# Kernel tuning notes

Hardware: AMD Instinct MI355X
Metric: run time of the kernel (lower is better)

The kernel has to match this reference:

```python
import jax, jax.numpy as jnp
import numpy as np


def _interp1d(xq, yq, xnew):
    """torchinterp1d semantics: linear interp with end-slope extrapolation.
    xq: (Q,) nondecreasing knots, yq: (Q,) values, xnew: any shape."""
    ind = jnp.clip(jnp.searchsorted(xq, xnew), 1, xq.shape[0] - 1)
    x0 = xq[ind - 1]
    x1 = xq[ind]
    y0 = yq[ind - 1]
    y1 = yq[ind]
    return y0 + (y1 - y0) / (x1 - x0) * (xnew - x0)


def setup_inputs() -> dict:
    key = jax.random.key(0)
    k1, k2 = jax.random.split(key)
    x = jax.random.normal(k1, (64, 512, 2048), dtype=jnp.float32)  # (N, C, L)
    target_quantiles = jax.random.uniform(k2, (256,), dtype=jnp.float32)  # sorted inside reference, as in the module
    return {"x": x, "target_quantiles": target_quantiles}


def reference(x, target_quantiles):
    # BatchOT forward (training=True, batchwise_matching=True, smoothing=None).
    C = x.shape[1]
    xt = jnp.moveaxis(x, 1, -1)        # (N, ..., C)
    flat = xt.reshape(-1, C)           # (M, C)
    Q = target_quantiles.shape[0]
    qs = jnp.linspace(0.0, 1.0, Q, dtype=x.dtype)      # buffer `quantiles`
    # per-feature batch quantiles, torch.quantile default 'linear' interpolation
    sq = jnp.quantile(flat, qs, axis=0)                # (Q, C)
    sq = jnp.sort(sq, axis=0)
    tq = jnp.sort(target_quantiles)
    # 1) map data through inverse source quantile fn, per feature: (M, C) -> [0,1]
    u = jax.vmap(_interp1d, in_axes=(1, None, 1), out_axes=1)(sq, qs, flat)
    u = jnp.clip(u, 0.0, 1.0)
    # 2) map quantile levels through the target quantile function (shared knots)
    y = _interp1d(qs, tq, u)           # (M, C)
    y = y.reshape(xt.shape)
    return jnp.moveaxis(y, -1, 1)      # (N, C, ...)
```

## Files before the change

kernel.cpp:

```cpp
#include <hip/hip_runtime.h>
#include <stdint.h>

#define N_   64
#define C_   512
#define L_   2048
#define M_   131072
#define Q_   256
#define NR_  512
#define NL_  (C_ * L_)
#define CAP_ 7168

__device__ __forceinline__ uint32_t f2u(float f) {
    uint32_t u = __float_as_uint(f);
    return u ^ ((uint32_t)((int32_t)u >> 31) | 0x80000000u);
}
__device__ __forceinline__ float u2f(uint32_t u) {
    uint32_t v = (u & 0x80000000u) ? (u ^ 0x80000000u) : ~u;
    return __uint_as_float(v);
}
__device__ __forceinline__ uint32_t h0pad(uint32_t b) { return b + (b >> 5); }

__global__ void sort_tq_kernel(const float* __restrict__ tq_in, float* __restrict__ tq_out) {
    __shared__ float s[Q_];
    int t = threadIdx.x;
    s[t] = tq_in[t];
    __syncthreads();
    for (int k = 2; k <= Q_; k <<= 1) {
        for (int j = k >> 1; j > 0; j >>= 1) {
            int ixj = t ^ j;
            if (ixj > t) {
                float a = s[t], b = s[ixj];
                bool up = ((t & k) == 0);
                if ((a > b) == up) { s[t] = b; s[ixj] = a; }
            }
            __syncthreads();
        }
    }
    tq_out[t] = s[t];
}

__device__ __forceinline__ uint32_t waveScan(uint32_t v, int lane) {
    #pragma unroll
    for (int off = 1; off < 64; off <<= 1) {
        uint32_t t = __shfl_up(v, off, 64);
        if (lane >= off) v += t;
    }
    return v;
}
__device__ __forceinline__ uint32_t blockScan(uint32_t v, uint32_t* wsum, int tid) {
    const int lane = tid & 63, wid = tid >> 6;
    uint32_t s = waveScan(v, lane);
    if (lane == 63) wsum[wid] = s;
    __syncthreads();
    if (wid == 0) {
        uint32_t w = (lane < 16) ? wsum[lane] : 0u;
        w = waveScan(w, lane);
        if (lane < 16) wsum[lane] = w;
    }
    __syncthreads();
    uint32_t r = s + ((wid > 0) ? wsum[wid - 1] : 0u);
    __syncthreads();
    return r;
}

__device__ __forceinline__ uint32_t dedupe512(uint32_t* keys, uint32_t* wsum, uint32_t* gout,
                                              uint32_t mykey, int tid, uint32_t* headOut) {
    if (tid < NR_) keys[tid] = mykey;
    __syncthreads();
    uint32_t h = 0;
    if (tid < NR_) h = (tid == 0) ? 1u : ((keys[tid] != keys[tid - 1]) ? 1u : 0u);
    uint32_t incl = blockScan(h, wsum, tid);
    if (tid == NR_ - 1) *gout = incl;
    *headOut = h;
    return incl - 1u;
}

__device__ __forceinline__ uint32_t rank_walk8(const uint32_t* rows, uint32_t slot, uint32_t& lrnk) {
    uint32_t acc = 0, dig = 0;
    bool found = false;
    const uint32_t* r = rows + slot * 17u;
    #pragma unroll
    for (int w = 0; w < 16; ++w) {
        uint32_t word = r[w];
        #pragma unroll
        for (int b = 0; b < 4; ++b) {
            uint32_t cnt = (word >> (8 * b)) & 255u;
            if (!found) {
                if (acc + cnt > lrnk) { dig = 4u * w + b; found = true; } else acc += cnt;
            }
        }
    }
    lrnk -= acc;
    return dig;
}

#define SM_KEYS 16896
#define SM_WSUM 17408
#define SM_M1   17424
#define SM_BS1  18448
#define SM_CNT2 18960
#define SM_BASE 19472
#define SM_GC   19984
#define SM_WORDS 19988

__global__ __launch_bounds__(1024, 8) void qsel_kernel(const float* __restrict__ x,
                                                       const float* __restrict__ tqs,
                                                       float* __restrict__ out) {
    __shared__ uint32_t smem[SM_WORDS];
    uint32_t* hist0   = smem;
    uint32_t* selBit  = smem;
    uint32_t* selBase = smem + 512;
    uint32_t* rows    = smem + 1024;
    uint32_t* candK   = smem + 1024;
    uint32_t* candS   = smem + 8192;
    float*    ssq     = (float*)(smem + 1024);
    float*    stq     = (float*)(smem + 1280);
    uint16_t* tbl16   = (uint16_t*)(smem + 2048);
    uint32_t* keys    = smem + SM_KEYS;
    uint32_t* wsum    = smem + SM_WSUM;
    uint2*    m1      = (uint2*)(smem + SM_M1);
    uint32_t* bs1     = smem + SM_BS1;
    uint32_t* cnt2    = smem + SM_CNT2;
    uint32_t* base    = smem + SM_BASE;
    uint32_t* gc      = smem + SM_GC;

    const int c = blockIdx.x, tid = threadIdx.x;
    const float* xc = x + (size_t)c * L_;
    float*       oc = out + (size_t)c * L_;
    const int l4 = (tid & 511) << 2;
    const int n0 = tid >> 9;

    uint32_t lrnk = 0;
    if (tid < NR_) {
        int k = tid >> 1;
        float pos = ((float)k / 255.0f) * 131071.0f;
        int lo = (int)floorf(pos);
        if (lo > M_ - 1) lo = M_ - 1;
        if (lo < 0) lo = 0;
        int r = (tid & 1) ? ((lo + 1 > M_ - 1) ? M_ - 1 : lo + 1) : lo;
        lrnk = (uint32_t)r;
    }

    for (int i = tid; i < 16896; i += 1024) hist0[i] = 0u;
    if (tid < 4) gc[tid] = 0u;
    __syncthreads();
    for (int nn = n0; nn < N_; nn += 8) {
        float4 a = *reinterpret_cast<const float4*>(xc + (size_t)nn       * NL_ + l4);
        float4 b = *reinterpret_cast<const float4*>(xc + (size_t)(nn + 2) * NL_ + l4);
        float4 d = *reinterpret_cast<const float4*>(xc + (size_t)(nn + 4) * NL_ + l4);
        float4 e = *reinterpret_cast<const float4*>(xc + (size_t)(nn + 6) * NL_ + l4);
        float vv[16] = {a.x,a.y,a.z,a.w, b.x,b.y,b.z,b.w, d.x,d.y,d.z,d.w, e.x,e.y,e.z,e.w};
        #pragma unroll
        for (int q = 0; q < 16; ++q)
            atomicAdd(&hist0[h0pad(f2u(vv[q]) >> 18)], 1u);
    }
    __syncthreads();

    {
        uint32_t bb = (uint32_t)tid * 16u; bb += (bb >> 5);
        uint32_t acc = 0;
        #pragma unroll
        for (int i = 0; i < 16; ++i) { acc += hist0[bb + i]; hist0[bb + i] = acc; }
        uint32_t excl = blockScan(acc, wsum, tid) - acc;
        #pragma unroll
        for (int i = 0; i < 16; ++i) hist0[bb + i] += excl;
    }
    __syncthreads();

    uint32_t mykey = 0;
    if (tid < NR_) {
        uint32_t d = 0;
        #pragma unroll
        for (uint32_t s = 8192; s > 0; s >>= 1)
            if (d + s <= 16384u && hist0[h0pad(d + s - 1u)] <= lrnk) d += s;
        uint32_t below = d ? hist0[h0pad(d - 1u)] : 0u;
        mykey = d;
        lrnk -= below;
    }
    __syncthreads();

    uint32_t head;
    uint32_t slot = dedupe512(keys, wsum, gc + 0, mykey, tid, &head);
    __syncthreads();

    if (tid < 512) { selBit[tid] = 0u; selBase[tid] = 0u; m1[tid] = make_uint2(0u, 0u); }
    for (int i = 1024 + tid; i < 9728; i += 1024) smem[i] = 0u;
    __syncthreads();
    if (tid < NR_ && head) atomicOr(&selBit[mykey >> 5], 1u << (mykey & 31u));
    __syncthreads();
    {
        uint32_t pc = (tid < 512) ? __popc(selBit[tid]) : 0u;
        uint32_t incl = blockScan(pc, wsum, tid);
        if (tid < 512) selBase[tid] = incl - pc;
    }
    __syncthreads();

    for (int nn = n0; nn < N_; nn += 8) {
        float4 a = *reinterpret_cast<const float4*>(xc + (size_t)nn       * NL_ + l4);
        float4 b = *reinterpret_cast<const float4*>(xc + (size_t)(nn + 2) * NL_ + l4);
        float4 d = *reinterpret_cast<const float4*>(xc + (size_t)(nn + 4) * NL_ + l4);
        float4 e = *reinterpret_cast<const float4*>(xc + (size_t)(nn + 6) * NL_ + l4);
        float vv[16] = {a.x,a.y,a.z,a.w, b.x,b.y,b.z,b.w, d.x,d.y,d.z,d.w, e.x,e.y,e.z,e.w};
        #pragma unroll
        for (int q = 0; q < 16; ++q) {
            uint32_t key = f2u(vv[q]);
            uint32_t bin = key >> 18;
            uint32_t w = selBit[bin >> 5];
            uint32_t bt = bin & 31u;
            if ((w >> bt) & 1u) {
                uint32_t slt = selBase[bin >> 5] + __popc(w & ((1u << bt) - 1u));
                uint32_t dd = (key >> 12) & 63u;
                atomicAdd(&rows[slt * 17u + (dd >> 2)], 1u << ((dd & 3u) << 3));
            }
        }
    }
    __syncthreads();

    uint32_t dig = 0;
    if (tid < NR_) { dig = rank_walk8(rows, slot, lrnk); mykey = (mykey << 6) | dig; }
    __syncthreads();
    uint32_t head1;
    uint32_t g1 = dedupe512(keys, wsum, gc + 1, mykey, tid, &head1);
    if (tid < NR_ && head1)
        atomicOr(&((uint32_t*)m1)[2u * slot + (dig >> 5)], 1u << (dig & 31u));
    if (tid == 0) gc[2] = 0u;
    if (tid < 512) cnt2[tid] = 0u;
    __syncthreads();
    {
        uint32_t S = gc[0];
        uint32_t pc = (tid < (int)S) ? (__popc(m1[tid].x) + __popc(m1[tid].y)) : 0u;
        uint32_t incl = blockScan(pc, wsum, tid);
        if (tid < 512) bs1[tid] = incl - pc;
    }
    __syncthreads();

    for (int nn = n0; nn < N_; nn += 8) {
        float4 a = *reinterpret_cast<const float4*>(xc + (size_t)nn       * NL_ + l4);
        float4 b = *reinterpret_cast<const float4*>(xc + (size_t)(nn + 2) * NL_ + l4);
        float4 d = *reinterpret_cast<const float4*>(xc + (size_t)(nn + 4) * NL_ + l4);
        float4 e = *reinterpret_cast<const float4*>(xc + (size_t)(nn + 6) * NL_ + l4);
        float vv[16] = {a.x,a.y,a.z,a.w, b.x,b.y,b.z,b.w, d.x,d.y,d.z,d.w, e.x,e.y,e.z,e.w};
        #pragma unroll
        for (int q = 0; q < 16; ++q) {
            uint32_t key = f2u(vv[q]);
            uint32_t bin = key >> 18;
            uint32_t w = selBit[bin >> 5];
            uint32_t bt = bin & 31u;
            if (!((w >> bt) & 1u)) continue;
            uint32_t slt = selBase[bin >> 5] + __popc(w & ((1u << bt) - 1u));
            uint2 mm = m1[slt];
            uint32_t dd = (key >> 12) & 63u;
            uint32_t mw = (dd < 32u) ? mm.x : mm.y;
            uint32_t db = dd & 31u;
            if (!((mw >> db) & 1u)) continue;
            uint32_t g = bs1[slt] + ((dd < 32u) ? __popc(mm.x & ((1u << db) - 1u))
                                                : __popc(mm.x) + __popc(mm.y & ((1u << db) - 1u)));
            uint32_t pos = atomicAdd(&gc[2], 1u);
            if (pos < CAP_) candK[pos] = key;
            atomicAdd(&cnt2[g], 1u);
        }
    }
    __syncthreads();

    uint32_t G1 = gc[1];
    uint32_t total = gc[2]; if (total > CAP_) total = CAP_;
    {
        uint32_t cv = (tid < (int)G1) ? cnt2[tid] : 0u;
        uint32_t incl = blockScan(cv, wsum, tid);
        if (tid < 512) { base[tid] = incl - cv; cnt2[tid] = 0u; }
    }
    __syncthreads();
    for (int i = tid; i < (int)total; i += 1024) {
        uint32_t key = candK[i];
        uint32_t bin = key >> 18;
        uint32_t w = selBit[bin >> 5];
        uint32_t bt = bin & 31u;
        uint32_t slt = selBase[bin >> 5] + __popc(w & ((1u << bt) - 1u));
        uint2 mm = m1[slt];
        uint32_t dd = (key >> 12) & 63u;
        uint32_t db = dd & 31u;
        uint32_t g = bs1[slt] + ((dd < 32u) ? __popc(mm.x & ((1u << db) - 1u))
                                            : __popc(mm.x) + __popc(mm.y & ((1u << db) - 1u)));
        uint32_t j = base[g] + atomicAdd(&cnt2[g], 1u);
        if (j < CAP_) candS[j] = key;
    }
    __syncthreads();

    uint32_t finalKey = 0;
    if (tid < NR_) {
        uint32_t b = base[g1];
        uint32_t n = ((g1 + 1u < G1) ? base[g1 + 1u] : total) - b;
        for (uint32_t i = 0; i < n; ++i) {
            uint32_t ki = candS[b + i];
            uint32_t clt = 0, ceq = 0;
            for (uint32_t j = 0; j < n; ++j) {
                uint32_t kj = candS[b + j];
                clt += (kj < ki) ? 1u : 0u;
                ceq += (kj == ki) ? 1u : 0u;
            }
            if (clt <= lrnk && lrnk < clt + ceq) { finalKey = ki; break; }
        }
    }
    __syncthreads();
    if (tid < NR_) keys[tid] = finalKey;
    __syncthreads();

    if (tid < Q_) {
        float pos = ((float)tid / 255.0f) * 131071.0f;
        float fr  = pos - floorf(pos);
        float vlo = u2f(keys[2 * tid]);
        float vhi = u2f(keys[2 * tid + 1]);
        ssq[tid] = vlo + fr * (vhi - vlo);
        stq[tid] = tqs[tid];
    }
    __syncthreads();
    for (int j = tid; j < 16384; j += 1024) {
        float edge = u2f((uint32_t)j << 18);
        uint32_t cnt = 0;
        #pragma unroll
        for (uint32_t s = 256; s > 0; s >>= 1)
            if (cnt + s <= 256u && ssq[cnt + s - 1] < edge) cnt += s;
        tbl16[j] = (uint16_t)cnt;
    }
    __syncthreads();

    for (int nn = n0; nn < N_; nn += 4) {
        const float4 a = *reinterpret_cast<const float4*>(xc + (size_t)nn       * NL_ + l4);
        const float4 b = *reinterpret_cast<const float4*>(xc + (size_t)(nn + 2) * NL_ + l4);
        float4 oa, ob;
        #pragma unroll
        for (int h = 0; h < 8; ++h) {
            float v = (h == 0) ? a.x : (h == 1) ? a.y : (h == 2) ? a.z : (h == 3) ? a.w
                    : (h == 4) ? b.x : (h == 5) ? b.y : (h == 6) ? b.z : b.w;
            uint32_t t = tbl16[f2u(v) >> 18];
            while (t < 256u && ssq[t] < v) ++t;
            uint32_t ind = (t < 1u) ? 1u : ((t > 255u) ? 255u : t);
            float x0 = ssq[ind - 1], x1 = ssq[ind];
            float r = (v - x0) / (x1 - x0);
            r = fminf(fmaxf(r, 0.0f), 1.0f);
            float y0 = stq[ind - 1], y1 = stq[ind];
            float y = y0 + (y1 - y0) * r;
            if      (h == 0) oa.x = y; else if (h == 1) oa.y = y;
            else if (h == 2) oa.z = y; else if (h == 3) oa.w = y;
            else if (h == 4) ob.x = y; else if (h == 5) ob.y = y;
            else if (h == 6) ob.z = y; else               ob.w = y;
        }
        *reinterpret_cast<float4*>(oc + (size_t)nn       * NL_ + l4) = oa;
        *reinterpret_cast<float4*>(oc + (size_t)(nn + 2) * NL_ + l4) = ob;
    }
}

extern "C" void kernel_launch(void* const* d_in, const int* in_sizes, int n_in,
                              void* d_out, int out_size, void* d_ws, size_t ws_size,
                              hipStream_t stream) {
    const float* x     = (const float*)d_in[0];
    const float* tq_in = (const float*)d_in[1];
    float* out = (float*)d_out;

    float* tqs = (float*)d_ws;

    sort_tq_kernel<<<1, Q_, 0, stream>>>(tq_in, tqs);
    qsel_kernel<<<C_, 1024, 0, stream>>>(x, tqs, out);
}
```

Baseline: 301.2 us.

## Build bucket table via histogram scan and precompute per-segment interpolation coefficients

Replaces the per-bucket binary search that built the 16K-entry lookup table with an atomic histogram of knot buckets followed by a block prefix scan, flagging buckets that contain knots so the linear probe runs only when needed. Per-segment interpolation data (x0, 1/dx, y0, dy) is packed into one float4 so each element does a single LDS read and a multiply instead of four reads and a divide. Multiplying by a reciprocal can differ slightly from dividing, and the shared-memory layout is rearranged to fit the new table.

```diff
diff --git a/kernel.cpp b/kernel.cpp
--- a/kernel.cpp
+++ b/kernel.cpp
@@ -114,8 +114,9 @@
     uint32_t* candK   = smem + 1024;
     uint32_t* candS   = smem + 8192;
     float*    ssq     = (float*)(smem + 1024);
-    float*    stq     = (float*)(smem + 1280);
-    uint16_t* tbl16   = (uint16_t*)(smem + 2048);
+    float4*   kt      = (float4*)(smem + 1280);
+    uint32_t* tblw    = smem + 2304;
+    uint16_t* tbl16   = (uint16_t*)(smem + 2304);
     uint32_t* keys    = smem + SM_KEYS;
     uint32_t* wsum    = smem + SM_WSUM;
     uint2*    m1      = (uint2*)(smem + SM_M1);
@@ -311,16 +312,38 @@
         float vlo = u2f(keys[2 * tid]);
         float vhi = u2f(keys[2 * tid + 1]);
         ssq[tid] = vlo + fr * (vhi - vlo);
-        stq[tid] = tqs[tid];
-    }
-    __syncthreads();
-    for (int j = tid; j < 16384; j += 1024) {
-        float edge = u2f((uint32_t)j << 18);
-        uint32_t cnt = 0;
-        #pragma unroll
-        for (uint32_t s = 256; s > 0; s >>= 1)
-            if (cnt + s <= 256u && ssq[cnt + s - 1] < edge) cnt += s;
-        tbl16[j] = (uint16_t)cnt;
+    }
+    for (int i = tid; i < 8192; i += 1024) tblw[i] = 0u;
+    __syncthreads();
+
+    if (tid < Q_) {
+        if (tid >= 1) {
+            float x0 = ssq[tid - 1], x1 = ssq[tid];
+            float y0 = tqs[tid - 1], y1 = tqs[tid];
+            float dx = x1 - x0;
+            kt[tid] = make_float4(x0, 1.0f / dx, y0, y1 - y0);
+        }
+        uint32_t kb = f2u(ssq[tid]) >> 18;
+        atomicAdd(&tblw[kb >> 1], 1u << ((kb & 1u) << 4));
+    }
+    __syncthreads();
+
+    {
+        uint32_t bw = (uint32_t)tid * 8u;
+        uint32_t w[8];
+        #pragma unroll
+        for (int i = 0; i < 8; ++i) w[i] = tblw[bw + i];
+        uint32_t sum = 0;
+        #pragma unroll
+        for (int i = 0; i < 8; ++i) sum += (w[i] & 0xFFFFu) + (w[i] >> 16);
+        uint32_t run = blockScan(sum, wsum, tid) - sum;
+        #pragma unroll
+        for (int i = 0; i < 8; ++i) {
+            uint32_t c0 = w[i] & 0xFFFFu, c1 = w[i] >> 16;
+            uint32_t e0 = run | (c0 ? 0x8000u : 0u); run += c0;
+            uint32_t e1 = run | (c1 ? 0x8000u : 0u); run += c1;
+            tblw[bw + i] = e0 | (e1 << 16);
+        }
     }
     __syncthreads();
 
@@ -332,14 +355,16 @@
         for (int h = 0; h < 8; ++h) {
             float v = (h == 0) ? a.x : (h == 1) ? a.y : (h == 2) ? a.z : (h == 3) ? a.w
                     : (h == 4) ? b.x : (h == 5) ? b.y : (h == 6) ? b.z : b.w;
-            uint32_t t = tbl16[f2u(v) >> 18];
-            while (t < 256u && ssq[t] < v) ++t;
+            uint32_t e = tbl16[f2u(v) >> 18];
+            uint32_t t = e & 0x7FFFu;
+            if (e & 0x8000u) {
+                while (t < 256u && ssq[t] < v) ++t;
+            }
             uint32_t ind = (t < 1u) ? 1u : ((t > 255u) ? 255u : t);
-            float x0 = ssq[ind - 1], x1 = ssq[ind];
-            float r = (v - x0) / (x1 - x0);
+            float4 k = kt[ind];
+            float r = (v - k.x) * k.y;
             r = fminf(fmaxf(r, 0.0f), 1.0f);
-            float y0 = stq[ind - 1], y1 = stq[ind];
-            float y = y0 + (y1 - y0) * r;
+            float y = k.z + k.w * r;
             if      (h == 0) oa.x = y; else if (h == 1) oa.y = y;
             else if (h == 2) oa.z = y; else if (h == 3) oa.w = y;
             else if (h == 4) ob.x = y; else if (h == 5) ob.y = y;
```

Result: faster. 283.5 us (-5.9%).
